# Performance work log

Measured on AMD Instinct MI355X. Metric: run time of the kernel, lower is better.

## Reference

```python
import jax, jax.numpy as jnp
import numpy as np

H = 256   # input_size
P = 256   # state_size
BATCH, L = 8, 4096
DT_MIN, DT_MAX = 1e-3, 1e-1
LN_EPS = 1e-5


def _hippo_params():
    # HiPPO-N matrix (num_blocks=1), eigendecomposition in numpy (float64 then cast)
    idx = np.arange(P, dtype=np.float64)
    s = np.sqrt(idx + 0.5)
    A = -np.outer(s, s)
    A = np.tril(A) - np.triu(A, 1)
    np.fill_diagonal(A, -0.5)
    ev, V = np.linalg.eig(A)
    order = np.argsort(ev.real)
    ev, V = ev[order], V[:, order]
    return ev, V


def setup_inputs() -> dict:
    key = jax.random.key(0)
    k_u, = jax.random.split(key, 1)
    ev, V = _hippo_params()
    rng = np.random.default_rng(0)
    log_lambda_real = np.log(-np.clip(ev.real, None, -1e-4)).astype(np.float32)
    lambda_imag = ev.imag.astype(np.float32)
    V_inv = np.linalg.inv(V)
    B_init = rng.standard_normal((P, H)) / np.sqrt(P)
    B_tilde = V_inv @ B_init.astype(np.complex128)
    C_init = rng.standard_normal((H, P)) / np.sqrt(P)
    C_tilde = C_init.astype(np.complex128) @ V
    log_delta = (rng.random(P) * (np.log(DT_MAX) - np.log(DT_MIN)) + np.log(DT_MIN)).astype(np.float32)
    return {
        "u": jax.random.normal(k_u, (BATCH, L, H), dtype=jnp.float32),
        "log_lambda_real": jnp.asarray(log_lambda_real),
        "lambda_imag": jnp.asarray(lambda_imag),
        "B_tilde_real": jnp.asarray(B_tilde.real, dtype=jnp.float32),
        "B_tilde_imag": jnp.asarray(B_tilde.imag, dtype=jnp.float32),
        "C_tilde_real": jnp.asarray(C_tilde.real, dtype=jnp.float32),
        "C_tilde_imag": jnp.asarray(C_tilde.imag, dtype=jnp.float32),
        "log_delta": jnp.asarray(log_delta),
        "gamma": jnp.ones((H,), dtype=jnp.float32),
        "beta": jnp.zeros((H,), dtype=jnp.float32),
    }


def _layernorm(x, gamma, beta):
    mu = jnp.mean(x, axis=-1, keepdims=True)
    var = jnp.mean(jnp.square(x - mu), axis=-1, keepdims=True)
    return (x - mu) * jax.lax.rsqrt(var + LN_EPS) * gamma + beta


def _ssm(h, log_lambda_real, lambda_imag, B_tilde_real, B_tilde_imag,
         C_tilde_real, C_tilde_imag, log_delta):
    # Continuous-time diagonal SSM params
    lam = -jnp.exp(log_lambda_real) + 1j * lambda_imag            # (P,) complex
    B_tilde = B_tilde_real + 1j * B_tilde_imag                     # (P,H)
    C_tilde = C_tilde_real + 1j * C_tilde_imag                     # (H,P)
    delta = jnp.exp(log_delta)                                     # (P,)
    # ZOH discretization (eq. 6 of the S5 paper)
    lambda_bar = jnp.exp(lam * delta)                              # (P,)
    B_bar = ((lambda_bar - 1.0) / lam)[:, None] * B_tilde          # (P,H)
    # Bu_k = B_bar @ u_k  ->  (B,L,P) complex
    Bu = jnp.einsum('blh,ph->blp', h.astype(jnp.complex64), B_bar.astype(jnp.complex64))
    # Parallel associative scan for x_k = lambda_bar * x_{k-1} + Bu_k
    a = jnp.broadcast_to(lambda_bar.astype(jnp.complex64), Bu.shape)
    def combine(c1, c2):
        a1, b1 = c1
        a2, b2 = c2
        return a1 * a2, a2 * b1 + b2
    _, xs = jax.lax.associative_scan(combine, (a, Bu), axis=1)     # (B,L,P)
    # Project back to real output: y = Re(C_tilde @ x)
    y = jnp.einsum('blp,hp->blh', xs, C_tilde.astype(jnp.complex64)).real
    return y


def reference(u, log_lambda_real, lambda_imag, B_tilde_real, B_tilde_imag,
              C_tilde_real, C_tilde_imag, log_delta, gamma, beta):
    # S5Block: pre-LayerNorm -> S5 SSM -> GELU -> residual
    h = _layernorm(u, gamma, beta)
    y = _ssm(h, log_lambda_real, lambda_imag, B_tilde_real, B_tilde_imag,
             C_tilde_real, C_tilde_imag, log_delta)
    return u + jax.nn.gelu(y)
```

## Files before the change

kernel.cpp:

```cpp
#include <hip/hip_runtime.h>
#include <math.h>

#define HDIM 256
#define PDIM 256
#define BATCH 8
#define LSEQ 4096
#define MTOT (BATCH * LSEQ)
#define NCHUNK 128
#define CHLEN 32

typedef __attribute__((ext_vector_type(8))) short bf16x8;
typedef __attribute__((ext_vector_type(4))) float f32x4;

__device__ __forceinline__ unsigned short f2bf(float f) {
    union { float f; unsigned int u; } v; v.f = f;
    unsigned int r = v.u + 0x7FFFu + ((v.u >> 16) & 1u);
    return (unsigned short)(r >> 16);
}
__device__ __forceinline__ float bf2f(unsigned int lo16) {
    union { unsigned int u; float f; } v; v.u = lo16 << 16;
    return v.f;
}

__global__ void params_k(const float* __restrict__ llr, const float* __restrict__ lim,
                         const float* __restrict__ ldl, float* __restrict__ par) {
    int p = threadIdx.x;
    float er = expf(llr[p]);
    float im = lim[p];
    float d  = expf(ldl[p]);
    float zr = -er * d, zi = im * d;
    float ea = expf(zr);
    float ar = ea * cosf(zi), ai = ea * sinf(zi);
    float dr = -er, di = im;
    float den = dr * dr + di * di;
    float nr = ar - 1.0f, ni = ai;
    float cr = (nr * dr + ni * di) / den;
    float ci = (ni * dr - nr * di) / den;
    float eC = expf((float)CHLEN * zr);
    float sC, cC;
    sincosf((float)CHLEN * zi, &sC, &cC);
    par[2 * p]           = ar;
    par[2 * p + 1]       = ai;
    par[512 + 2 * p]     = cr;
    par[512 + 2 * p + 1] = ci;
    par[1024 + 2 * p]     = eC * cC;
    par[1024 + 2 * p + 1] = eC * sC;
}

__global__ void w1_k(const float* __restrict__ Br, const float* __restrict__ Bi,
                     const float* __restrict__ par, unsigned short* __restrict__ W1t) {
    int p = blockIdx.x, h = threadIdx.x;
    float cr = par[512 + 2 * p], ci = par[512 + 2 * p + 1];
    float br = Br[p * HDIM + h], bi = Bi[p * HDIM + h];
    W1t[(2 * p) * HDIM + h]     = f2bf(cr * br - ci * bi);
    W1t[(2 * p + 1) * HDIM + h] = f2bf(cr * bi + ci * br);
}

__global__ void w2_k(const float* __restrict__ Cr, const float* __restrict__ Ci,
                     unsigned short* __restrict__ W2t) {
    int p = blockIdx.x, h = threadIdx.x;
    W2t[h * (2 * PDIM) + 2 * p]     = f2bf(Cr[h * PDIM + p]);
    W2t[h * (2 * PDIM) + 2 * p + 1] = f2bf(-Ci[h * PDIM + p]);
}

__global__ void ln_k(const float* __restrict__ u, unsigned short* __restrict__ hbf,
                     const float* __restrict__ gamma, const float* __restrict__ beta) {
    __shared__ float gS[HDIM], bS[HDIM];
    int t = threadIdx.x;
    gS[t] = gamma[t]; bS[t] = beta[t];
    int lane = t & 63, wv = t >> 6;
    int row = blockIdx.x * 4 + wv;
    float4 v = *(const float4*)(u + (size_t)row * HDIM + lane * 4);
    float s  = v.x + v.y + v.z + v.w;
    float sq = v.x * v.x + v.y * v.y + v.z * v.z + v.w * v.w;
    #pragma unroll
    for (int o = 1; o < 64; o <<= 1) { s += __shfl_xor(s, o); sq += __shfl_xor(sq, o); }
    float mu = s * (1.0f / HDIM);
    float rs = rsqrtf(sq * (1.0f / HDIM) - mu * mu + 1e-5f);
    __syncthreads();
    int c = lane * 4;
    ushort4 o;
    o.x = f2bf((v.x - mu) * rs * gS[c + 0] + bS[c + 0]);
    o.y = f2bf((v.y - mu) * rs * gS[c + 1] + bS[c + 1]);
    o.z = f2bf((v.z - mu) * rs * gS[c + 2] + bS[c + 2]);
    o.w = f2bf((v.w - mu) * rs * gS[c + 3] + bS[c + 3]);
    *(ushort4*)(hbf + (size_t)row * HDIM + c) = o;
}

#define LDK 40

template <int MODE>
__launch_bounds__(256, 2)
__global__ void mfma_gemm_k(const unsigned short* __restrict__ A,
                            const unsigned short* __restrict__ B,
                            void* __restrict__ outv,
                            const float* __restrict__ u,
                            int N, int K) {
    __shared__ unsigned short As[128 * LDK];
    __shared__ unsigned short Bs[128 * LDK];
    const int t = threadIdx.x;
    const int bn = blockIdx.x, bm = blockIdx.y;
    const int lane = t & 63;
    const int wm = ((t >> 6) & 1) * 64;
    const int wn = ((t >> 6) >> 1) * 64;
    const int srow = t >> 1, skoff = (t & 1) * 16;
    const unsigned short* Ap = A + (size_t)(bm * 128 + srow) * K + skoff;
    const unsigned short* Bp = B + (size_t)(bn * 128 + srow) * K + skoff;
    unsigned short* AsW = &As[srow * LDK + skoff];
    unsigned short* BsW = &Bs[srow * LDK + skoff];
    const int mrow = lane & 15;
    const int kq = (lane >> 4) * 8;

    f32x4 acc[4][4] = {};

    for (int k0 = 0; k0 < K; k0 += 32) {
        uint4 a0 = *(const uint4*)(Ap + k0);
        uint4 a1 = *(const uint4*)(Ap + k0 + 8);
        uint4 b0 = *(const uint4*)(Bp + k0);
        uint4 b1 = *(const uint4*)(Bp + k0 + 8);
        __syncthreads();
        *(uint4*)AsW       = a0;
        *(uint4*)(AsW + 8) = a1;
        *(uint4*)BsW       = b0;
        *(uint4*)(BsW + 8) = b1;
        __syncthreads();
        bf16x8 fa[4], fb[4];
        #pragma unroll
        for (int i = 0; i < 4; i++) {
            fa[i] = *(const bf16x8*)&As[(wm + i * 16 + mrow) * LDK + kq];
            fb[i] = *(const bf16x8*)&Bs[(wn + i * 16 + mrow) * LDK + kq];
        }
        #pragma unroll
        for (int i = 0; i < 4; i++)
            #pragma unroll
            for (int j = 0; j < 4; j++)
                acc[i][j] = __builtin_amdgcn_mfma_f32_16x16x32_bf16(fa[i], fb[j], acc[i][j], 0, 0, 0);
    }

    const int r0 = (lane >> 4) * 4;
    const int c0 = lane & 15;
    #pragma unroll
    for (int i = 0; i < 4; i++) {
        #pragma unroll
        for (int r = 0; r < 4; r++) {
            const size_t rowoff = (size_t)(bm * 128 + wm + i * 16 + r0 + r) * N;
            #pragma unroll
            for (int j = 0; j < 4; j++) {
                const int col_g = bn * 128 + wn + j * 16 + c0;
                float y = acc[i][j][r];
                if (MODE == 0) {
                    ((unsigned short*)outv)[rowoff + col_g] = f2bf(y);
                } else {
                    float z = 0.7978845608f * fmaf(0.044715f * y * y, y, y);
                    float e = __expf(2.0f * z);
                    float th = 1.0f - 2.0f / (e + 1.0f);
                    float g = 0.5f * y * (1.0f + th);
                    ((float*)outv)[rowoff + col_g] = u[rowoff + col_g] + g;
                }
            }
        }
    }
}

__global__ void scan_reduce_k(const unsigned short* __restrict__ Bu,
                              const float* __restrict__ par, float* __restrict__ last) {
    int p = threadIdx.x, c = blockIdx.x, b = blockIdx.y;
    float ar = par[2 * p], ai = par[2 * p + 1];
    float xr = 0.0f, xi = 0.0f;
    const unsigned int* q = (const unsigned int*)(Bu + ((size_t)b * LSEQ + (size_t)c * CHLEN) * 512) + p;
    #pragma unroll 8
    for (int j = 0; j < CHLEN; j++) {
        unsigned int v = q[j * 256];
        float vr = bf2f(v & 0xFFFFu), vi = bf2f(v >> 16);
        float nr = fmaf(ar, xr, fmaf(-ai, xi, vr));
        float ni = fmaf(ar, xi, fmaf(ai, xr, vi));
        xr = nr; xi = ni;
    }
    *(float2*)(last + ((size_t)b * NCHUNK + c) * 512 + 2 * p) = make_float2(xr, xi);
}

__global__ void scan_carry_k(const float* __restrict__ last, float* __restrict__ prefix,
                             const float* __restrict__ par) {
    int p = threadIdx.x, b = blockIdx.x;
    float Ar = par[1024 + 2 * p], Ai = par[1024 + 2 * p + 1];
    float Pr = 0.0f, Pi = 0.0f;
    for (int c = 0; c < NCHUNK; c++) {
        size_t idx = ((size_t)b * NCHUNK + c) * 512 + 2 * p;
        *(float2*)(prefix + idx) = make_float2(Pr, Pi);
        float2 l = *(const float2*)(last + idx);
        float nr = fmaf(Ar, Pr, fmaf(-Ai, Pi, l.x));
        float ni = fmaf(Ar, Pi, fmaf(Ai, Pr, l.y));
        Pr = nr; Pi = ni;
    }
}

__global__ void scan_apply_k(unsigned short* __restrict__ Bu, const float* __restrict__ par,
                             const float* __restrict__ prefix) {
    int p = threadIdx.x, c = blockIdx.x, b = blockIdx.y;
    float ar = par[2 * p], ai = par[2 * p + 1];
    float2 P = *(const float2*)(prefix + ((size_t)b * NCHUNK + c) * 512 + 2 * p);
    float xr = P.x, xi = P.y;
    unsigned int* q = (unsigned int*)(Bu + ((size_t)b * LSEQ + (size_t)c * CHLEN) * 512) + p;
    #pragma unroll 8
    for (int j = 0; j < CHLEN; j++) {
        unsigned int v = q[j * 256];
        float vr = bf2f(v & 0xFFFFu), vi = bf2f(v >> 16);
        float nr = fmaf(ar, xr, fmaf(-ai, xi, vr));
        float ni = fmaf(ar, xi, fmaf(ai, xr, vi));
        xr = nr; xi = ni;
        q[j * 256] = (unsigned int)f2bf(xr) | ((unsigned int)f2bf(xi) << 16);
    }
}

extern "C" void kernel_launch(void* const* d_in, const int* in_sizes, int n_in,
                              void* d_out, int out_size, void* d_ws, size_t ws_size,
                              hipStream_t stream) {
    const float* u   = (const float*)d_in[0];
    const float* llr = (const float*)d_in[1];
    const float* lim = (const float*)d_in[2];
    const float* Br  = (const float*)d_in[3];
    const float* Bi  = (const float*)d_in[4];
    const float* Cr  = (const float*)d_in[5];
    const float* Ci  = (const float*)d_in[6];
    const float* ldl = (const float*)d_in[7];
    const float* gam = (const float*)d_in[8];
    const float* bet = (const float*)d_in[9];
    float* out = (float*)d_out;

    float* ws     = (float*)d_ws;
    float* par    = ws;
    float* last   = ws + 2048;
    float* prefix = last + (size_t)BATCH * NCHUNK * 512;
    unsigned short* W1t = (unsigned short*)(prefix + (size_t)BATCH * NCHUNK * 512);
    unsigned short* W2t = W1t + 512 * HDIM;
    unsigned short* hbf = W2t + HDIM * 512;
    unsigned short* Bu  = hbf + (size_t)MTOT * HDIM;

    params_k<<<1, PDIM, 0, stream>>>(llr, lim, ldl, par);
    w1_k<<<PDIM, HDIM, 0, stream>>>(Br, Bi, par, W1t);
    w2_k<<<PDIM, HDIM, 0, stream>>>(Cr, Ci, W2t);
    ln_k<<<MTOT / 4, 256, 0, stream>>>(u, hbf, gam, bet);

    mfma_gemm_k<0><<<dim3(512 / 128, MTOT / 128), 256, 0, stream>>>(
        hbf, W1t, (void*)Bu, nullptr, 512, HDIM);

    scan_reduce_k<<<dim3(NCHUNK, BATCH), PDIM, 0, stream>>>(Bu, par, last);
    scan_carry_k<<<BATCH, PDIM, 0, stream>>>(last, prefix, par);
    scan_apply_k<<<dim3(NCHUNK, BATCH), PDIM, 0, stream>>>(Bu, par, prefix);

    mfma_gemm_k<1><<<dim3(HDIM / 128, MTOT / 128), 256, 0, stream>>>(
        Bu, W2t, (void*)out, u, HDIM, 512);
}
```

Measured before the change: 173.9 us.

## Use direct global-to-LDS loads with XOR swizzle, tile remap, and merged weight prep

The GEMM kernel now loads A and B tiles straight into LDS with global_load_lds, using an XOR-swizzled unpadded layout in place of padded register staging. It also remaps workgroups to tiles so neighbouring blocks share operand rows, and makes K a template constant. The W1/W2 prep kernels are merged into one kernel that recomputes the discretization parameters itself, and scan_carry batches 16 loads ahead of its serial recurrence. The aim is to cut register staging, bank conflicts and launch count, at the cost of a more complex swizzle that must match between the write and read sides.

Result: faster. 165.3 us (-4.9%).

```diff
diff --git a/kernel.cpp b/kernel.cpp
--- a/kernel.cpp
+++ b/kernel.cpp
@@ -20,6 +20,12 @@
 __device__ __forceinline__ float bf2f(unsigned int lo16) {
     union { unsigned int u; float f; } v; v.u = lo16 << 16;
     return v.f;
+}
+
+__device__ __forceinline__ void gload_lds16(const void* g, void* l) {
+    __builtin_amdgcn_global_load_lds(
+        (const __attribute__((address_space(1))) void*)g,
+        (__attribute__((address_space(3))) void*)l, 16, 0, 0);
 }
 
 __global__ void params_k(const float* __restrict__ llr, const float* __restrict__ lim,
@@ -47,20 +53,34 @@
     par[1024 + 2 * p + 1] = eC * sC;
 }
 
-__global__ void w1_k(const float* __restrict__ Br, const float* __restrict__ Bi,
-                     const float* __restrict__ par, unsigned short* __restrict__ W1t) {
-    int p = blockIdx.x, h = threadIdx.x;
-    float cr = par[512 + 2 * p], ci = par[512 + 2 * p + 1];
-    float br = Br[p * HDIM + h], bi = Bi[p * HDIM + h];
-    W1t[(2 * p) * HDIM + h]     = f2bf(cr * br - ci * bi);
-    W1t[(2 * p + 1) * HDIM + h] = f2bf(cr * bi + ci * br);
-}
-
-__global__ void w2_k(const float* __restrict__ Cr, const float* __restrict__ Ci,
-                     unsigned short* __restrict__ W2t) {
-    int p = blockIdx.x, h = threadIdx.x;
-    W2t[h * (2 * PDIM) + 2 * p]     = f2bf(Cr[h * PDIM + p]);
-    W2t[h * (2 * PDIM) + 2 * p + 1] = f2bf(-Ci[h * PDIM + p]);
+__global__ void wpack_k(const float* __restrict__ llr, const float* __restrict__ lim,
+                        const float* __restrict__ ldl,
+                        const float* __restrict__ Br, const float* __restrict__ Bi,
+                        const float* __restrict__ Cr, const float* __restrict__ Ci,
+                        unsigned short* __restrict__ W1t, unsigned short* __restrict__ W2t) {
+    int h = threadIdx.x;
+    if (blockIdx.x < PDIM) {
+        int p = blockIdx.x;
+        float er = expf(llr[p]);
+        float im = lim[p];
+        float d  = expf(ldl[p]);
+        float zr = -er * d, zi = im * d;
+        float ea = expf(zr);
+        float sz, cz; sincosf(zi, &sz, &cz);
+        float ar = ea * cz, ai = ea * sz;
+        float dr = -er, di = im;
+        float den = dr * dr + di * di;
+        float nr = ar - 1.0f, ni = ai;
+        float cr = (nr * dr + ni * di) / den;
+        float ci = (ni * dr - nr * di) / den;
+        float br = Br[p * HDIM + h], bi = Bi[p * HDIM + h];
+        W1t[(2 * p) * HDIM + h]     = f2bf(cr * br - ci * bi);
+        W1t[(2 * p + 1) * HDIM + h] = f2bf(cr * bi + ci * br);
+    } else {
+        int p = blockIdx.x - PDIM;
+        W2t[h * (2 * PDIM) + 2 * p]     = f2bf(Cr[h * PDIM + p]);
+        W2t[h * (2 * PDIM) + 2 * p + 1] = f2bf(-Ci[h * PDIM + p]);
+    }
 }
 
 __global__ void ln_k(const float* __restrict__ u, unsigned short* __restrict__ hbf,
@@ -87,48 +107,55 @@
     *(ushort4*)(hbf + (size_t)row * HDIM + c) = o;
 }
 
-#define LDK 40
-
-template <int MODE>
+template <int MODE, int K>
 __launch_bounds__(256, 2)
 __global__ void mfma_gemm_k(const unsigned short* __restrict__ A,
                             const unsigned short* __restrict__ B,
                             void* __restrict__ outv,
                             const float* __restrict__ u,
-                            int N, int K) {
-    __shared__ unsigned short As[128 * LDK];
-    __shared__ unsigned short Bs[128 * LDK];
+                            int N) {
+    __shared__ __align__(16) unsigned short As[128 * 32];
+    __shared__ __align__(16) unsigned short Bs[128 * 32];
     const int t = threadIdx.x;
-    const int bn = blockIdx.x, bm = blockIdx.y;
-    const int lane = t & 63;
-    const int wm = ((t >> 6) & 1) * 64;
-    const int wn = ((t >> 6) >> 1) * 64;
-    const int srow = t >> 1, skoff = (t & 1) * 16;
-    const unsigned short* Ap = A + (size_t)(bm * 128 + srow) * K + skoff;
-    const unsigned short* Bp = B + (size_t)(bn * 128 + srow) * K + skoff;
-    unsigned short* AsW = &As[srow * LDK + skoff];
-    unsigned short* BsW = &Bs[srow * LDK + skoff];
+
+    const int nbn  = (int)gridDim.x;
+    const int flat = (int)blockIdx.y * nbn + (int)blockIdx.x;
+    const int nwg  = nbn * (int)gridDim.y;
+    const int tile = (flat & 7) * (nwg >> 3) + (flat >> 3);
+    const int bn = tile % nbn, bm = tile / nbn;
+
+    const int lane = t & 63, w = t >> 6;
+
+    const int srow   = 32 * w + (lane >> 2);
+    const int schunk = (lane & 3) ^ ((lane >> 3) & 3);
+    const unsigned short* gA = A + (size_t)(bm * 128 + srow) * K + schunk * 8;
+    const unsigned short* gB = B + (size_t)(bn * 128 + srow) * K + schunk * 8;
+    unsigned short* lA0 = &As[(32 * w) * 32];
+    unsigned short* lA1 = &As[(32 * w + 16) * 32];
+    unsigned short* lB0 = &Bs[(32 * w) * 32];
+    unsigned short* lB1 = &Bs[(32 * w + 16) * 32];
+
+    const int wm = (w & 1) * 64;
+    const int wn = (w >> 1) * 64;
     const int mrow = lane & 15;
-    const int kq = (lane >> 4) * 8;
+    const int rsw  = (mrow >> 1) & 3;
+    const int cch  = lane >> 4;
+    const int fcol = ((cch ^ rsw) * 8);
 
     f32x4 acc[4][4] = {};
 
     for (int k0 = 0; k0 < K; k0 += 32) {
-        uint4 a0 = *(const uint4*)(Ap + k0);
-        uint4 a1 = *(const uint4*)(Ap + k0 + 8);
-        uint4 b0 = *(const uint4*)(Bp + k0);
-        uint4 b1 = *(const uint4*)(Bp + k0 + 8);
         __syncthreads();
-        *(uint4*)AsW       = a0;
-        *(uint4*)(AsW + 8) = a1;
-        *(uint4*)BsW       = b0;
-        *(uint4*)(BsW + 8) = b1;
+        gload_lds16(gA + k0,          lA0);
+        gload_lds16(gA + 16 * K + k0, lA1);
+        gload_lds16(gB + k0,          lB0);
+        gload_lds16(gB + 16 * K + k0, lB1);
         __syncthreads();
         bf16x8 fa[4], fb[4];
         #pragma unroll
         for (int i = 0; i < 4; i++) {
-            fa[i] = *(const bf16x8*)&As[(wm + i * 16 + mrow) * LDK + kq];
-            fb[i] = *(const bf16x8*)&Bs[(wn + i * 16 + mrow) * LDK + kq];
+            fa[i] = *(const bf16x8*)&As[(wm + i * 16 + mrow) * 32 + fcol];
+            fb[i] = *(const bf16x8*)&Bs[(wn + i * 16 + mrow) * 32 + fcol];
         }
         #pragma unroll
         for (int i = 0; i < 4; i++)
@@ -184,13 +211,19 @@
     int p = threadIdx.x, b = blockIdx.x;
     float Ar = par[1024 + 2 * p], Ai = par[1024 + 2 * p + 1];
     float Pr = 0.0f, Pi = 0.0f;
-    for (int c = 0; c < NCHUNK; c++) {
-        size_t idx = ((size_t)b * NCHUNK + c) * 512 + 2 * p;
-        *(float2*)(prefix + idx) = make_float2(Pr, Pi);
-        float2 l = *(const float2*)(last + idx);
-        float nr = fmaf(Ar, Pr, fmaf(-Ai, Pi, l.x));
-        float ni = fmaf(Ar, Pi, fmaf(Ai, Pr, l.y));
-        Pr = nr; Pi = ni;
+    const float2* lp = (const float2*)(last + (size_t)b * NCHUNK * 512) + p;
+    float2* pp = (float2*)(prefix + (size_t)b * NCHUNK * 512) + p;
+    for (int c0 = 0; c0 < NCHUNK; c0 += 16) {
+        float2 v[16];
+        #pragma unroll
+        for (int j = 0; j < 16; j++) v[j] = lp[(size_t)(c0 + j) * 256];
+        #pragma unroll
+        for (int j = 0; j < 16; j++) {
+            pp[(size_t)(c0 + j) * 256] = make_float2(Pr, Pi);
+            float nr = fmaf(Ar, Pr, fmaf(-Ai, Pi, v[j].x));
+            float ni = fmaf(Ar, Pi, fmaf(Ai, Pr, v[j].y));
+            Pr = nr; Pi = ni;
+        }
     }
 }
 
@@ -236,18 +269,17 @@
     unsigned short* hbf = W2t + HDIM * 512;
     unsigned short* Bu  = hbf + (size_t)MTOT * HDIM;
 
+    ln_k<<<MTOT / 4, 256, 0, stream>>>(u, hbf, gam, bet);
+    wpack_k<<<2 * PDIM, HDIM, 0, stream>>>(llr, lim, ldl, Br, Bi, Cr, Ci, W1t, W2t);
     params_k<<<1, PDIM, 0, stream>>>(llr, lim, ldl, par);
-    w1_k<<<PDIM, HDIM, 0, stream>>>(Br, Bi, par, W1t);
-    w2_k<<<PDIM, HDIM, 0, stream>>>(Cr, Ci, W2t);
-    ln_k<<<MTOT / 4, 256, 0, stream>>>(u, hbf, gam, bet);
-
-    mfma_gemm_k<0><<<dim3(512 / 128, MTOT / 128), 256, 0, stream>>>(
-        hbf, W1t, (void*)Bu, nullptr, 512, HDIM);
+
+    mfma_gemm_k<0, HDIM><<<dim3(512 / 128, MTOT / 128), 256, 0, stream>>>(
+        hbf, W1t, (void*)Bu, nullptr, 512);
 
     scan_reduce_k<<<dim3(NCHUNK, BATCH), PDIM, 0, stream>>>(Bu, par, last);
     scan_carry_k<<<BATCH, PDIM, 0, stream>>>(last, prefix, par);
     scan_apply_k<<<dim3(NCHUNK, BATCH), PDIM, 0, stream>>>(Bu, par, prefix);
 
-    mfma_gemm_k<1><<<dim3(HDIM / 128, MTOT / 128), 256, 0, stream>>>(
-        Bu, W2t, (void*)out, u, HDIM, 512);
-}
+    mfma_gemm_k<1, 512><<<dim3(HDIM / 128, MTOT / 128), 256, 0, stream>>>(
+        Bu, W2t, (void*)out, u, HDIM);
+}
```
